# Performance work log

Hardware: AMD Instinct MI355X
Metric: run time of the kernel (lower is better)

Reference implementation:

```python
import jax, jax.numpy as jnp
import numpy as np

NUM_T = 1000   # num_timesteps == timesteps -> skip = 1, seq = range(0, 1000)
ETA = 0.1
BETA_START, BETA_END = 1e-4, 0.02


def _ddim_schedule():
    # get_beta_schedule: linspace in float64, then cast
    betas = np.linspace(BETA_START, BETA_END, NUM_T, dtype=np.float64)
    # compute_alpha prepends beta=0 -> alpha_cumprod[0] = 1.0, indexed at t+1
    alph = np.concatenate([[1.0], np.cumprod(1.0 - betas)]).astype(np.float32)
    seq = np.arange(NUM_T)
    seq_next = np.concatenate([[-1], seq[:-1]])
    at = alph[seq + 1]
    at_next = alph[seq_next + 1]   # t=-1 -> alph[0] = 1.0
    # loop iterates reversed(seq) x reversed(seq_next)
    return (jnp.asarray(at[::-1].copy()),
            jnp.asarray(at_next[::-1].copy()),
            jnp.asarray(seq[::-1].copy(), dtype=jnp.int32))


def setup_inputs() -> dict:
    key = jax.random.key(0)
    k1, k2, k3, k4, k5 = jax.random.split(key, 5)
    n, c, s, h, w = 2, 3, 8, 64, 44
    return {
        "skes": jax.random.normal(k1, (n, c, s, h, w), dtype=jnp.float32),
        "sil_T": jax.random.normal(k2, (n * s, 1, h, w), dtype=jnp.float32),
        "w_skes": jax.random.normal(k3, (c,), dtype=jnp.float32),
        "w_sil": jax.random.normal(k4, (), dtype=jnp.float32),
        "t_scale": jax.random.normal(k5, (), dtype=jnp.float32),
    }


def reference(skes, sil_T, w_skes, w_sil, t_scale):
    n, c, s, h, w = skes.shape
    # rearrange 'n c s h w -> (n s) c h w'
    skes2 = jnp.transpose(skes, (0, 2, 1, 3, 4)).reshape(n * s, c, h, w)
    # surrogate denoiser condition: 1x1 channel projection of the skeleton maps
    cond = jnp.einsum('nchw,c->nhw', skes2, w_skes)[:, None]  # (n*s,1,h,w)
    at_r, atn_r, idx_r = _ddim_schedule()
    noise_key = jax.random.key(42)

    def model(sil_t, t_val):
        t_emb = t_scale * (t_val.astype(jnp.float32) / NUM_T)
        return jnp.tanh(cond + w_sil * sil_t + t_emb)

    def step(sil_t, x):
        at, atn, idx = x
        sil_0 = model(sil_t, idx)
        # NOTE: original uses the FIXED initial noise sil_T here (not sil_t)
        et = (sil_T - jnp.sqrt(at) * sil_0) / jnp.sqrt(1.0 - at)
        c1 = ETA * jnp.sqrt((1.0 - at / atn) * (1.0 - atn) / (1.0 - at))
        c2 = jnp.sqrt(jnp.maximum(1.0 - atn - c1 * c1, 0.0))
        noise = jax.random.normal(jax.random.fold_in(noise_key, idx),
                                  sil_T.shape, dtype=sil_T.dtype)
        sil_next = jnp.sqrt(atn) * sil_0 + c1 * noise + c2 * et
        return sil_next, sil_0

    _, preds = jax.lax.scan(step, sil_T, (at_r, atn_r, idx_r))
    # preds: (1000, n*s, 1, h, w) == stacked list of per-step sil_0 predictions
    return preds
```

## Files before the change

kernel.cpp:

```cpp
#include <hip/hip_runtime.h>
#include <cstdint>

#define NSTEP 1000
#define NELEM 45056
#define HW    2816
#define EPB   64
#define PW    8
#define BLK   ((PW + 1) * 64)
#define WIN   40
#define SPP   (WIN / PW)
#define NWIN  (NSTEP / WIN)

struct AlphTab { float a[NSTEP + 1]; };

constexpr AlphTab make_alph() {
    AlphTab t{};
    t.a[0] = 1.0f;
    double alph = 1.0;
    const double start = 1e-4, stop = 0.02;
    const double step = (stop - start) / 999.0;
    for (int i = 0; i < NSTEP; ++i) {
        double beta = (i == NSTEP - 1) ? stop : ((double)i * step + start);
        alph *= (1.0 - beta);
        t.a[i + 1] = (float)alph;
    }
    return t;
}
constexpr AlphTab ALPH = make_alph();

__device__ __forceinline__ void tf20(uint32_t K0, uint32_t K1, uint32_t K2,
                                     uint32_t& x0, uint32_t& x1) {
    x0 += K0; x1 += K1;
#define TFR(r) { x0 += x1; x1 = ((x1 << r) | (x1 >> (32 - r))); x1 ^= x0; }
    TFR(13) TFR(15) TFR(26) TFR(6)
    x0 += K1; x1 += K2 + 1u;
    TFR(17) TFR(29) TFR(16) TFR(24)
    x0 += K2; x1 += K0 + 2u;
    TFR(13) TFR(15) TFR(26) TFR(6)
    x0 += K0; x1 += K1 + 3u;
    TFR(17) TFR(29) TFR(16) TFR(24)
    x0 += K1; x1 += K2 + 4u;
    TFR(13) TFR(15) TFR(26) TFR(6)
    x0 += K2; x1 += K0 + 5u;
#undef TFR
}

__device__ __forceinline__ float bits_to_erfinv(uint32_t bits) {
    const float f2 = __uint_as_float((bits >> 9) | 0x3F800000u) - 1.0f;
    const float u  = f2 * 2.0f - 0.99999994f;
    const float t1 = (1.0f - u) * (1.0f + u);
    const float w  = __log2f(t1) * -0.6931472f;
    const bool  lt = w < 5.0f;

    const float wwn = w - 2.5f;
    float pn =           2.81022636e-08f;
    pn = fmaf(pn, wwn,   3.43273939e-07f);
    pn = fmaf(pn, wwn,  -3.5233877e-06f);
    pn = fmaf(pn, wwn,  -4.39150654e-06f);
    pn = fmaf(pn, wwn,   0.00021858087f);
    pn = fmaf(pn, wwn,  -0.00125372503f);
    pn = fmaf(pn, wwn,  -0.00417768164f);
    pn = fmaf(pn, wwn,   0.246640727f);
    pn = fmaf(pn, wwn,   1.50140941f);

    float p = pn;
    if (__any(!lt)) {
        const float sw  = __builtin_amdgcn_sqrtf(w);
        const float wwf = sw - 3.0f;
        float pf =           -0.000200214257f;
        pf = fmaf(pf, wwf,    0.000100950558f);
        pf = fmaf(pf, wwf,    0.00134934322f);
        pf = fmaf(pf, wwf,   -0.00367342844f);
        pf = fmaf(pf, wwf,    0.00573950773f);
        pf = fmaf(pf, wwf,   -0.0076224613f);
        pf = fmaf(pf, wwf,    0.00943887047f);
        pf = fmaf(pf, wwf,    1.00167406f);
        pf = fmaf(pf, wwf,    2.83297682f);
        p = lt ? pn : pf;
    }
    return p * u;
}

__global__ __launch_bounds__(BLK)
void fused_kernel(const float* __restrict__ skes,
                  const float* __restrict__ silT,
                  const float* __restrict__ wskes,
                  const float* __restrict__ wsil_p,
                  const float* __restrict__ tsc_p,
                  float* __restrict__ out) {
    __shared__ __align__(16) uint4    tabP[NSTEP];
    __shared__            uint32_t    tabK2[NSTEP];
    __shared__ __align__(8)  uint2    tabC[NSTEP];
    __shared__ __align__(16) float    dbuf[2][WIN][EPB];

    const float wsil = wsil_p[0];
    const float tsc  = tsc_p[0];
    const float L2E2 = 2.8853900817779268f;

    for (int k = (int)threadIdx.x; k < NSTEP; k += BLK) {
        const int t = 999 - k;
        const float at  = ALPH.a[t + 1];
        const float atn = ALPH.a[t];
        const float c1 = 0.1f * sqrtf((1.0f - at / atn) * (1.0f - atn) / (1.0f - at));
        const float c2 = sqrtf(fmaxf(1.0f - atn - c1 * c1, 0.0f));
        const float rs = 1.0f / sqrtf(1.0f - at);
        const float A  = sqrtf(atn) - c2 * sqrtf(at) * rs;
        const float e  = c2 * rs;
        const float temb = tsc * ((float)t / 1000.0f);
        uint32_t k0 = 0u, k1 = (uint32_t)t;
        tf20(0u, 42u, 0x1BD11BDAu ^ 42u, k0, k1);
        tabP[k]  = make_uint4(__float_as_uint(c1 * 1.4142135f),
                              __float_as_uint(e), k0, k1);
        tabK2[k] = k0 ^ k1 ^ 0x1BD11BDAu;
        tabC[k]  = make_uint2(__float_as_uint(A), __float_as_uint(temb * L2E2));
    }

    const int wid  = (int)(threadIdx.x >> 6);
    const int lane = (int)(threadIdx.x & 63);
    const int j    = (int)(blockIdx.x * EPB) + lane;

    const float sT = silT[j];

    float cc2 = 0.0f, ws2 = 0.0f, sil = 0.0f;
    if (wid == PW) {
        const int ns = j / HW;
        const int hw = j - ns * HW;
        const int n  = ns >> 3;
        const int ss = ns & 7;
        const float* sk = skes + (size_t)((n * 3) * 8 + ss) * HW + hw;
        const float w0 = wskes[0], w1 = wskes[1], w2 = wskes[2];
        const float cond = fmaf(w2, sk[2 * 8 * HW], fmaf(w1, sk[8 * HW], w0 * sk[0]));
        cc2 = cond * L2E2;
        ws2 = wsil * L2E2;
        sil = sT;
    }

    __syncthreads();

    if (wid < PW) {
        float* db = &dbuf[0][0][0];
#pragma unroll
        for (int s = 0; s < SPP; ++s) {
            const int kk = wid + s * PW;
            const uint4 ta    = tabP[kk];
            const uint32_t k2 = tabK2[kk];
            uint32_t x0 = 0u, x1 = (uint32_t)j;
            tf20(ta.z, ta.w, k2, x0, x1);
            const float ei = bits_to_erfinv(x0 ^ x1);
            db[kk * EPB + lane] =
                fmaf(__uint_as_float(ta.x), ei, __uint_as_float(ta.y) * sT);
        }
    }
    __syncthreads();

    float* op = out + j;

    for (int w = 0; w < NWIN; ++w) {
        if (wid < PW) {
            if (w + 1 < NWIN) {
                float* db = &dbuf[(w + 1) & 1][0][0];
                const int kbase = (w + 1) * WIN;
#pragma unroll
                for (int s = 0; s < SPP; ++s) {
                    const int kk = wid + s * PW;
                    const int k  = kbase + kk;
                    const uint4 ta    = tabP[k];
                    const uint32_t k2 = tabK2[k];
                    uint32_t x0 = 0u, x1 = (uint32_t)j;
                    tf20(ta.z, ta.w, k2, x0, x1);
                    const float ei = bits_to_erfinv(x0 ^ x1);
                    db[kk * EPB + lane] =
                        fmaf(__uint_as_float(ta.x), ei, __uint_as_float(ta.y) * sT);
                }
            }
        } else {
            const float* db = &dbuf[w & 1][0][0];
            const int kbase = w * WIN;
#pragma unroll 4
            for (int kk = 0; kk < WIN; ++kk) {
                const uint2 tt = tabC[kbase + kk];
                const float A  = __uint_as_float(tt.x);
                const float tb = __uint_as_float(tt.y);
                const float e2 = __builtin_amdgcn_exp2f(fmaf(ws2, sil, cc2 + tb));
                const float r  = __builtin_amdgcn_rcpf(e2 + 1.0f);
                const float s0 = fmaf(-2.0f, r, 1.0f);
                *op = s0; op += NELEM;
                sil = fmaf(A, s0, db[kk * EPB + lane]);
            }
        }
        __syncthreads();
    }
}

extern "C" void kernel_launch(void* const* d_in, const int* in_sizes, int n_in,
                              void* d_out, int out_size, void* d_ws, size_t ws_size,
                              hipStream_t stream) {
    const float* skes = (const float*)d_in[0];
    const float* silT = (const float*)d_in[1];
    const float* wsk  = (const float*)d_in[2];
    const float* wsil = (const float*)d_in[3];
    const float* tsc  = (const float*)d_in[4];
    float* out = (float*)d_out;
    (void)in_sizes; (void)n_in; (void)out_size; (void)d_ws; (void)ws_size;

    dim3 grid(NELEM / EPB), block(BLK);
    hipLaunchKernelGGL(fused_kernel, grid, block, 0, stream,
                       skes, silT, wsk, wsil, tsc, out);
}
```

Measured before the change: 321.4 us.

## Replace windowed barrier pipeline with flag-based producer-consumer ring buffer

The block-wide __syncthreads double-buffered windows are replaced by a 64-slot shared-memory ring. Eight producer waves publish per-step flags, and the consumer wave polls those flags with a ballot and advances a shared consumer position. This removes barrier stalls where the serial consumer wave waits for the slowest producer, or the reverse, at every window boundary. Producers get raised priority and the tabK2 table is dropped in favour of recomputing the key. The cost is spin-wait polling, s_sleep latency, and relying on volatile LDS accesses plus block fences for ordering.

```diff
diff --git a/kernel.cpp b/kernel.cpp
--- a/kernel.cpp
+++ b/kernel.cpp
@@ -7,9 +7,7 @@
 #define EPB   64
 #define PW    8
 #define BLK   ((PW + 1) * 64)
-#define WIN   40
-#define SPP   (WIN / PW)
-#define NWIN  (NSTEP / WIN)
+#define RING  64
 
 struct AlphTab { float a[NSTEP + 1]; };
 
@@ -89,9 +87,10 @@
                   const float* __restrict__ tsc_p,
                   float* __restrict__ out) {
     __shared__ __align__(16) uint4    tabP[NSTEP];
-    __shared__            uint32_t    tabK2[NSTEP];
     __shared__ __align__(8)  uint2    tabC[NSTEP];
-    __shared__ __align__(16) float    dbuf[2][WIN][EPB];
+    __shared__ __align__(16) float    dbuf[RING][EPB];
+    __shared__ uint32_t               flags[RING];
+    __shared__ uint32_t               consPos;
 
     const float wsil = wsil_p[0];
     const float tsc  = tsc_p[0];
@@ -111,9 +110,10 @@
         tf20(0u, 42u, 0x1BD11BDAu ^ 42u, k0, k1);
         tabP[k]  = make_uint4(__float_as_uint(c1 * 1.4142135f),
                               __float_as_uint(e), k0, k1);
-        tabK2[k] = k0 ^ k1 ^ 0x1BD11BDAu;
         tabC[k]  = make_uint2(__float_as_uint(A), __float_as_uint(temb * L2E2));
     }
+    if (threadIdx.x < RING) flags[threadIdx.x] = 0u;
+    if (threadIdx.x == 0)   consPos = 0u;
 
     const int wid  = (int)(threadIdx.x >> 6);
     const int lane = (int)(threadIdx.x & 63);
@@ -138,57 +138,57 @@
     __syncthreads();
 
     if (wid < PW) {
-        float* db = &dbuf[0][0][0];
-#pragma unroll
-        for (int s = 0; s < SPP; ++s) {
-            const int kk = wid + s * PW;
-            const uint4 ta    = tabP[kk];
-            const uint32_t k2 = tabK2[kk];
-            uint32_t x0 = 0u, x1 = (uint32_t)j;
-            tf20(ta.z, ta.w, k2, x0, x1);
-            const float ei = bits_to_erfinv(x0 ^ x1);
-            db[kk * EPB + lane] =
-                fmaf(__uint_as_float(ta.x), ei, __uint_as_float(ta.y) * sT);
-        }
-    }
-    __syncthreads();
-
-    float* op = out + j;
-
-    for (int w = 0; w < NWIN; ++w) {
-        if (wid < PW) {
-            if (w + 1 < NWIN) {
-                float* db = &dbuf[(w + 1) & 1][0][0];
-                const int kbase = (w + 1) * WIN;
-#pragma unroll
-                for (int s = 0; s < SPP; ++s) {
-                    const int kk = wid + s * PW;
-                    const int k  = kbase + kk;
-                    const uint4 ta    = tabP[k];
-                    const uint32_t k2 = tabK2[k];
-                    uint32_t x0 = 0u, x1 = (uint32_t)j;
-                    tf20(ta.z, ta.w, k2, x0, x1);
-                    const float ei = bits_to_erfinv(x0 ^ x1);
-                    db[kk * EPB + lane] =
-                        fmaf(__uint_as_float(ta.x), ei, __uint_as_float(ta.y) * sT);
+        __builtin_amdgcn_s_setprio(1);
+        volatile uint32_t* vcons = &consPos;
+        int cached = 0;
+#pragma unroll 1
+        for (int k = wid; k < NSTEP; k += PW) {
+            if (k >= RING) {
+                const int need = k - RING + 1;
+                while (cached < need) {
+                    cached = (int)*vcons;
+                    if (cached < need) __builtin_amdgcn_s_sleep(1);
                 }
             }
-        } else {
-            const float* db = &dbuf[w & 1][0][0];
-            const int kbase = w * WIN;
-#pragma unroll 4
-            for (int kk = 0; kk < WIN; ++kk) {
-                const uint2 tt = tabC[kbase + kk];
+            const uint4 ta = tabP[k];
+            uint32_t x0 = 0u, x1 = (uint32_t)j;
+            tf20(ta.z, ta.w, ta.z ^ ta.w ^ 0x1BD11BDAu, x0, x1);
+            const float ei = bits_to_erfinv(x0 ^ x1);
+            dbuf[k & (RING - 1)][lane] =
+                fmaf(__uint_as_float(ta.x), ei, __uint_as_float(ta.y) * sT);
+            __threadfence_block();
+            if (lane == 0)
+                ((volatile uint32_t*)flags)[k & (RING - 1)] = (uint32_t)(k + 1);
+        }
+    } else {
+        volatile uint32_t* vflags = flags;
+        float* op = out + j;
+        int k = 0;
+        while (k < NSTEP) {
+            const int kl = k + lane;
+            bool ready = true;
+            if (kl < NSTEP)
+                ready = (vflags[kl & (RING - 1)] == (uint32_t)(kl + 1));
+            const unsigned long long m = __ballot(ready);
+            int run = (~m == 0ull) ? 64 : (__ffsll((unsigned long long)~m) - 1);
+            if (run <= 0) { __builtin_amdgcn_s_sleep(1); continue; }
+            if (run > NSTEP - k) run = NSTEP - k;
+#pragma unroll 1
+            for (int i = 0; i < run; ++i) {
+                const float d  = dbuf[(k + i) & (RING - 1)][lane];
+                const uint2 tt = tabC[k + i];
                 const float A  = __uint_as_float(tt.x);
                 const float tb = __uint_as_float(tt.y);
                 const float e2 = __builtin_amdgcn_exp2f(fmaf(ws2, sil, cc2 + tb));
                 const float r  = __builtin_amdgcn_rcpf(e2 + 1.0f);
                 const float s0 = fmaf(-2.0f, r, 1.0f);
                 *op = s0; op += NELEM;
-                sil = fmaf(A, s0, db[kk * EPB + lane]);
+                sil = fmaf(A, s0, d);
             }
+            k += run;
+            __threadfence_block();
+            if (lane == 0) *((volatile uint32_t*)&consPos) = (uint32_t)k;
         }
-        __syncthreads();
     }
 }
 
```

New measurement: 435.6 us. 1.36x slower.

## Replace block barriers with LDS counter-based producer/consumer handoff between waves

Applied to the files above, without the earlier changes.

Removes the per-window __syncthreads. Producer waves now signal window completion through atomic counters in shared memory, and the consumer wave publishes its progress position, giving asynchronous double-buffered flow control. Producers get raised scheduling priority, the K2 table is dropped in favour of recomputation, and the consumer batches LDS loads in groups of four. It relies on LDS spin-waits with volatile accesses and compiler-only memory fences, which risks ordering bugs across waves and adds spin overhead.

```diff
diff --git a/kernel.cpp b/kernel.cpp
--- a/kernel.cpp
+++ b/kernel.cpp
@@ -10,6 +10,7 @@
 #define WIN   40
 #define SPP   (WIN / PW)
 #define NWIN  (NSTEP / WIN)
+#define NBUF  2
 
 struct AlphTab { float a[NSTEP + 1]; };
 
@@ -89,9 +90,10 @@
                   const float* __restrict__ tsc_p,
                   float* __restrict__ out) {
     __shared__ __align__(16) uint4    tabP[NSTEP];
-    __shared__            uint32_t    tabK2[NSTEP];
     __shared__ __align__(8)  uint2    tabC[NSTEP];
-    __shared__ __align__(16) float    dbuf[2][WIN][EPB];
+    __shared__ __align__(16) float    dbuf[NBUF][WIN][EPB];
+    __shared__ uint32_t               wincnt[NWIN];
+    __shared__ uint32_t               consPos;
 
     const float wsil = wsil_p[0];
     const float tsc  = tsc_p[0];
@@ -111,9 +113,10 @@
         tf20(0u, 42u, 0x1BD11BDAu ^ 42u, k0, k1);
         tabP[k]  = make_uint4(__float_as_uint(c1 * 1.4142135f),
                               __float_as_uint(e), k0, k1);
-        tabK2[k] = k0 ^ k1 ^ 0x1BD11BDAu;
         tabC[k]  = make_uint2(__float_as_uint(A), __float_as_uint(temb * L2E2));
     }
+    if (threadIdx.x < NWIN) wincnt[threadIdx.x] = 0u;
+    if (threadIdx.x == 0)   consPos = 0u;
 
     const int wid  = (int)(threadIdx.x >> 6);
     const int lane = (int)(threadIdx.x & 63);
@@ -138,57 +141,65 @@
     __syncthreads();
 
     if (wid < PW) {
-        float* db = &dbuf[0][0][0];
-#pragma unroll
-        for (int s = 0; s < SPP; ++s) {
-            const int kk = wid + s * PW;
-            const uint4 ta    = tabP[kk];
-            const uint32_t k2 = tabK2[kk];
-            uint32_t x0 = 0u, x1 = (uint32_t)j;
-            tf20(ta.z, ta.w, k2, x0, x1);
-            const float ei = bits_to_erfinv(x0 ^ x1);
-            db[kk * EPB + lane] =
-                fmaf(__uint_as_float(ta.x), ei, __uint_as_float(ta.y) * sT);
+        __builtin_amdgcn_s_setprio(1);
+        volatile uint32_t* vcons = &consPos;
+#pragma unroll 1
+        for (int w = 0; w < NWIN; ++w) {
+            if (w >= NBUF) {
+                const uint32_t need = (uint32_t)(w - NBUF + 1);
+                while (*vcons < need) __builtin_amdgcn_s_sleep(2);
+            }
+            const int kbase = w * WIN + wid;
+            uint4 tt[SPP];
+#pragma unroll
+            for (int s = 0; s < SPP; ++s) tt[s] = tabP[kbase + s * PW];
+            float* db = &dbuf[w & (NBUF - 1)][0][0];
+#pragma unroll
+            for (int s = 0; s < SPP; ++s) {
+                uint32_t x0 = 0u, x1 = (uint32_t)j;
+                tf20(tt[s].z, tt[s].w, tt[s].z ^ tt[s].w ^ 0x1BD11BDAu, x0, x1);
+                const float ei = bits_to_erfinv(x0 ^ x1);
+                db[(wid + s * PW) * EPB + lane] =
+                    fmaf(__uint_as_float(tt[s].x), ei,
+                         __uint_as_float(tt[s].y) * sT);
+            }
+            asm volatile("" ::: "memory");
+            if (lane == 0) atomicAdd(&wincnt[w], 1u);
+            asm volatile("" ::: "memory");
         }
-    }
-    __syncthreads();
-
-    float* op = out + j;
-
-    for (int w = 0; w < NWIN; ++w) {
-        if (wid < PW) {
-            if (w + 1 < NWIN) {
-                float* db = &dbuf[(w + 1) & 1][0][0];
-                const int kbase = (w + 1) * WIN;
-#pragma unroll
-                for (int s = 0; s < SPP; ++s) {
-                    const int kk = wid + s * PW;
-                    const int k  = kbase + kk;
-                    const uint4 ta    = tabP[k];
-                    const uint32_t k2 = tabK2[k];
-                    uint32_t x0 = 0u, x1 = (uint32_t)j;
-                    tf20(ta.z, ta.w, k2, x0, x1);
-                    const float ei = bits_to_erfinv(x0 ^ x1);
-                    db[kk * EPB + lane] =
-                        fmaf(__uint_as_float(ta.x), ei, __uint_as_float(ta.y) * sT);
+    } else {
+        volatile uint32_t* vwin  = wincnt;
+        volatile uint32_t* vcons = &consPos;
+        float* op = out + j;
+#pragma unroll 1
+        for (int w = 0; w < NWIN; ++w) {
+            while (vwin[w] < (uint32_t)PW) __builtin_amdgcn_s_sleep(1);
+            asm volatile("" ::: "memory");
+            const float* db = &dbuf[w & (NBUF - 1)][0][0];
+            const int kbase = w * WIN;
+#pragma unroll 1
+            for (int g = 0; g < WIN / 4; ++g) {
+                float d4[4]; uint2 t4[4];
+#pragma unroll
+                for (int i = 0; i < 4; ++i) {
+                    d4[i] = db[(g * 4 + i) * EPB + lane];
+                    t4[i] = tabC[kbase + g * 4 + i];
+                }
+#pragma unroll
+                for (int i = 0; i < 4; ++i) {
+                    const float A  = __uint_as_float(t4[i].x);
+                    const float tb = __uint_as_float(t4[i].y);
+                    const float e2 = __builtin_amdgcn_exp2f(fmaf(ws2, sil, cc2 + tb));
+                    const float r  = __builtin_amdgcn_rcpf(e2 + 1.0f);
+                    const float s0 = fmaf(-2.0f, r, 1.0f);
+                    *op = s0; op += NELEM;
+                    sil = fmaf(A, s0, d4[i]);
                 }
             }
-        } else {
-            const float* db = &dbuf[w & 1][0][0];
-            const int kbase = w * WIN;
-#pragma unroll 4
-            for (int kk = 0; kk < WIN; ++kk) {
-                const uint2 tt = tabC[kbase + kk];
-                const float A  = __uint_as_float(tt.x);
-                const float tb = __uint_as_float(tt.y);
-                const float e2 = __builtin_amdgcn_exp2f(fmaf(ws2, sil, cc2 + tb));
-                const float r  = __builtin_amdgcn_rcpf(e2 + 1.0f);
-                const float s0 = fmaf(-2.0f, r, 1.0f);
-                *op = s0; op += NELEM;
-                sil = fmaf(A, s0, db[kk * EPB + lane]);
-            }
+            asm volatile("" ::: "memory");
+            *vcons = (uint32_t)(w + 1);
+            asm volatile("" ::: "memory");
         }
-        __syncthreads();
     }
 }
 
```

Result: slower. 349.6 us (+8.8%).

## Move step tables to a setup kernel in workspace and shrink producer warps

Applied to the files above, without the earlier changes.

A separate setup kernel now precomputes the per-step coefficient and RNG-key tables into global workspace, so each block no longer rebuilds them in shared memory. That frees most of the LDS, which together with 7 producer waves and a launch-bounds occupancy hint is meant to let more blocks run per CU. The consumer wave batches its loads of 8 buffer entries and table values before running the serial tanh chain, and a monolithic fallback kernel is added for when the workspace is too small. The cost is an extra kernel launch and global or cache reads of the tables in place of LDS reads.

```diff
diff --git a/kernel.cpp b/kernel.cpp
--- a/kernel.cpp
+++ b/kernel.cpp
@@ -5,11 +5,13 @@
 #define NELEM 45056
 #define HW    2816
 #define EPB   64
-#define PW    8
+#define PW    7
 #define BLK   ((PW + 1) * 64)
 #define WIN   40
-#define SPP   (WIN / PW)
 #define NWIN  (NSTEP / WIN)
+#define NBUF  2
+#define TABC_OFF 16384
+#define WS_NEED  (TABC_OFF + NSTEP * 8)
 
 struct AlphTab { float a[NSTEP + 1]; };
 
@@ -45,6 +47,12 @@
 #undef TFR
 }
 
+__device__ __forceinline__ float fast_tanh(float x) {
+    const float e2 = __expf(x + x);
+    const float r  = __builtin_amdgcn_rcpf(e2 + 1.0f);
+    return fmaf(-2.0f, r, 1.0f);
+}
+
 __device__ __forceinline__ float bits_to_erfinv(uint32_t bits) {
     const float f2 = __uint_as_float((bits >> 9) | 0x3F800000u) - 1.0f;
     const float u  = f2 * 2.0f - 0.99999994f;
@@ -81,23 +89,127 @@
     return p * u;
 }
 
-__global__ __launch_bounds__(BLK)
+__global__ __launch_bounds__(256)
+void setup_kernel(const float* __restrict__ tsc_p,
+                  uint4* __restrict__ tabPg, uint2* __restrict__ tabCg) {
+    const int k = (int)(blockIdx.x * 256u + threadIdx.x);
+    if (k >= NSTEP) return;
+    const float tsc = tsc_p[0];
+    const float L2E2 = 2.8853900817779268f;
+    const int t = 999 - k;
+    const float at  = ALPH.a[t + 1];
+    const float atn = ALPH.a[t];
+    const float c1 = 0.1f * sqrtf((1.0f - at / atn) * (1.0f - atn) / (1.0f - at));
+    const float c2 = sqrtf(fmaxf(1.0f - atn - c1 * c1, 0.0f));
+    const float rs = 1.0f / sqrtf(1.0f - at);
+    const float A  = sqrtf(atn) - c2 * sqrtf(at) * rs;
+    const float e  = c2 * rs;
+    const float temb = tsc * ((float)t / 1000.0f);
+    uint32_t k0 = 0u, k1 = (uint32_t)t;
+    tf20(0u, 42u, 0x1BD11BDAu ^ 42u, k0, k1);
+    tabPg[k] = make_uint4(__float_as_uint(c1 * 1.4142135f),
+                          __float_as_uint(e), k0, k1);
+    tabCg[k] = make_uint2(__float_as_uint(A), __float_as_uint(temb * L2E2));
+}
+
+__device__ __forceinline__ void produce_window(const uint4* __restrict__ tabPg,
+                                               float* __restrict__ db,
+                                               int kbase, int wid, int lane,
+                                               int j, float sT) {
+    const int ks0 = __builtin_amdgcn_readfirstlane(kbase + wid);
+#pragma unroll 2
+    for (int s = 0, kk = wid; kk < WIN; ++s, kk += PW) {
+        const uint4 ta = tabPg[ks0 + s * PW];
+        uint32_t x0 = 0u, x1 = (uint32_t)j;
+        tf20(ta.z, ta.w, ta.z ^ ta.w ^ 0x1BD11BDAu, x0, x1);
+        const float ei = bits_to_erfinv(x0 ^ x1);
+        db[kk * EPB + lane] =
+            fmaf(__uint_as_float(ta.x), ei, __uint_as_float(ta.y) * sT);
+    }
+}
+
+__global__ __launch_bounds__(BLK, 8)
 void fused_kernel(const float* __restrict__ skes,
                   const float* __restrict__ silT,
                   const float* __restrict__ wskes,
                   const float* __restrict__ wsil_p,
-                  const float* __restrict__ tsc_p,
+                  const uint4* __restrict__ tabPg,
+                  const uint2* __restrict__ tabCg,
                   float* __restrict__ out) {
-    __shared__ __align__(16) uint4    tabP[NSTEP];
-    __shared__            uint32_t    tabK2[NSTEP];
-    __shared__ __align__(8)  uint2    tabC[NSTEP];
-    __shared__ __align__(16) float    dbuf[2][WIN][EPB];
-
+    __shared__ __align__(16) float dbuf[NBUF][WIN][EPB];
+
+    const int wid  = (int)(threadIdx.x >> 6);
+    const int lane = (int)(threadIdx.x & 63);
+    const int j    = (int)(blockIdx.x * EPB) + lane;
+
+    const float sT = silT[j];
+
+    float cc2 = 0.0f, ws2 = 0.0f, sil = 0.0f;
+    if (wid == PW) {
+        const float L2E2 = 2.8853900817779268f;
+        const int ns = j / HW;
+        const int hw = j - ns * HW;
+        const int n  = ns >> 3;
+        const int ss = ns & 7;
+        const float* sk = skes + (size_t)((n * 3) * 8 + ss) * HW + hw;
+        const float w0 = wskes[0], w1 = wskes[1], w2 = wskes[2];
+        const float cond = fmaf(w2, sk[2 * 8 * HW], fmaf(w1, sk[8 * HW], w0 * sk[0]));
+        cc2 = cond * L2E2;
+        ws2 = wsil_p[0] * L2E2;
+        sil = sT;
+    }
+
+    if (wid < PW) {
+        produce_window(tabPg, &dbuf[0][0][0], 0, wid, lane, j, sT);
+    }
+    __syncthreads();
+
+    float* op = out + j;
+
+    for (int w = 0; w < NWIN; ++w) {
+        if (wid < PW) {
+            if (w + 1 < NWIN) {
+                produce_window(tabPg, &dbuf[(w + 1) & (NBUF - 1)][0][0],
+                               (w + 1) * WIN, wid, lane, j, sT);
+            }
+        } else {
+            const float* db = &dbuf[w & (NBUF - 1)][0][0];
+            const int ks0 = __builtin_amdgcn_readfirstlane(w * WIN);
+#pragma unroll 1
+            for (int g = 0; g < WIN / 8; ++g) {
+                float d8[8]; uint2 t8[8];
+#pragma unroll
+                for (int i = 0; i < 8; ++i) {
+                    d8[i] = db[(g * 8 + i) * EPB + lane];
+                    t8[i] = tabCg[ks0 + g * 8 + i];
+                }
+#pragma unroll
+                for (int i = 0; i < 8; ++i) {
+                    const float A  = __uint_as_float(t8[i].x);
+                    const float tb = __uint_as_float(t8[i].y);
+                    const float e2 = __builtin_amdgcn_exp2f(fmaf(ws2, sil, cc2 + tb));
+                    const float r  = __builtin_amdgcn_rcpf(e2 + 1.0f);
+                    const float s0 = fmaf(-2.0f, r, 1.0f);
+                    *op = s0; op += NELEM;
+                    sil = fmaf(A, s0, d8[i]);
+                }
+            }
+        }
+        __syncthreads();
+    }
+}
+
+__global__ __launch_bounds__(256)
+void diffgait_mono(const float* __restrict__ skes,
+                   const float* __restrict__ silT,
+                   const float* __restrict__ wskes,
+                   const float* __restrict__ wsil_p,
+                   const float* __restrict__ tsc_p,
+                   float* __restrict__ out) {
+    __shared__ __align__(16) uint32_t tab[NSTEP][8];
     const float wsil = wsil_p[0];
     const float tsc  = tsc_p[0];
-    const float L2E2 = 2.8853900817779268f;
-
-    for (int k = (int)threadIdx.x; k < NSTEP; k += BLK) {
+    for (int k = (int)threadIdx.x; k < NSTEP; k += 256) {
         const int t = 999 - k;
         const float at  = ALPH.a[t + 1];
         const float atn = ALPH.a[t];
@@ -107,88 +219,40 @@
         const float A  = sqrtf(atn) - c2 * sqrtf(at) * rs;
         const float e  = c2 * rs;
         const float temb = tsc * ((float)t / 1000.0f);
-        uint32_t k0 = 0u, k1 = (uint32_t)t;
-        tf20(0u, 42u, 0x1BD11BDAu ^ 42u, k0, k1);
-        tabP[k]  = make_uint4(__float_as_uint(c1 * 1.4142135f),
-                              __float_as_uint(e), k0, k1);
-        tabK2[k] = k0 ^ k1 ^ 0x1BD11BDAu;
-        tabC[k]  = make_uint2(__float_as_uint(A), __float_as_uint(temb * L2E2));
-    }
-
-    const int wid  = (int)(threadIdx.x >> 6);
-    const int lane = (int)(threadIdx.x & 63);
-    const int j    = (int)(blockIdx.x * EPB) + lane;
-
+        uint32_t x0 = 0u, x1 = (uint32_t)t;
+        tf20(0u, 42u, 0x1BD11BDAu ^ 42u, x0, x1);
+        tab[k][0] = __float_as_uint(A);
+        tab[k][1] = __float_as_uint(temb);
+        tab[k][2] = __float_as_uint(c1 * 1.4142135f);
+        tab[k][3] = __float_as_uint(e);
+        tab[k][4] = x0;
+        tab[k][5] = x1;
+        tab[k][6] = x0 ^ x1 ^ 0x1BD11BDAu;
+        tab[k][7] = 0u;
+    }
+    __syncthreads();
+    const int j  = (int)(blockIdx.x * 256u + threadIdx.x);
+    const int ns = j / HW;
+    const int hw = j - ns * HW;
+    const int n  = ns >> 3;
+    const int ss = ns & 7;
+    const float* sk = skes + (size_t)((n * 3) * 8 + ss) * HW + hw;
+    const float w0 = wskes[0], w1 = wskes[1], w2 = wskes[2];
+    const float cond = fmaf(w2, sk[2 * 8 * HW], fmaf(w1, sk[8 * HW], w0 * sk[0]));
     const float sT = silT[j];
-
-    float cc2 = 0.0f, ws2 = 0.0f, sil = 0.0f;
-    if (wid == PW) {
-        const int ns = j / HW;
-        const int hw = j - ns * HW;
-        const int n  = ns >> 3;
-        const int ss = ns & 7;
-        const float* sk = skes + (size_t)((n * 3) * 8 + ss) * HW + hw;
-        const float w0 = wskes[0], w1 = wskes[1], w2 = wskes[2];
-        const float cond = fmaf(w2, sk[2 * 8 * HW], fmaf(w1, sk[8 * HW], w0 * sk[0]));
-        cc2 = cond * L2E2;
-        ws2 = wsil * L2E2;
-        sil = sT;
-    }
-
-    __syncthreads();
-
-    if (wid < PW) {
-        float* db = &dbuf[0][0][0];
-#pragma unroll
-        for (int s = 0; s < SPP; ++s) {
-            const int kk = wid + s * PW;
-            const uint4 ta    = tabP[kk];
-            const uint32_t k2 = tabK2[kk];
-            uint32_t x0 = 0u, x1 = (uint32_t)j;
-            tf20(ta.z, ta.w, k2, x0, x1);
-            const float ei = bits_to_erfinv(x0 ^ x1);
-            db[kk * EPB + lane] =
-                fmaf(__uint_as_float(ta.x), ei, __uint_as_float(ta.y) * sT);
-        }
-    }
-    __syncthreads();
-
+    float sil = sT;
     float* op = out + j;
-
-    for (int w = 0; w < NWIN; ++w) {
-        if (wid < PW) {
-            if (w + 1 < NWIN) {
-                float* db = &dbuf[(w + 1) & 1][0][0];
-                const int kbase = (w + 1) * WIN;
-#pragma unroll
-                for (int s = 0; s < SPP; ++s) {
-                    const int kk = wid + s * PW;
-                    const int k  = kbase + kk;
-                    const uint4 ta    = tabP[k];
-                    const uint32_t k2 = tabK2[k];
-                    uint32_t x0 = 0u, x1 = (uint32_t)j;
-                    tf20(ta.z, ta.w, k2, x0, x1);
-                    const float ei = bits_to_erfinv(x0 ^ x1);
-                    db[kk * EPB + lane] =
-                        fmaf(__uint_as_float(ta.x), ei, __uint_as_float(ta.y) * sT);
-                }
-            }
-        } else {
-            const float* db = &dbuf[w & 1][0][0];
-            const int kbase = w * WIN;
-#pragma unroll 4
-            for (int kk = 0; kk < WIN; ++kk) {
-                const uint2 tt = tabC[kbase + kk];
-                const float A  = __uint_as_float(tt.x);
-                const float tb = __uint_as_float(tt.y);
-                const float e2 = __builtin_amdgcn_exp2f(fmaf(ws2, sil, cc2 + tb));
-                const float r  = __builtin_amdgcn_rcpf(e2 + 1.0f);
-                const float s0 = fmaf(-2.0f, r, 1.0f);
-                *op = s0; op += NELEM;
-                sil = fmaf(A, s0, db[kk * EPB + lane]);
-            }
-        }
-        __syncthreads();
+#pragma unroll 2
+    for (int k = 0; k < NSTEP; ++k) {
+        const uint4 ta = *(const uint4*)&tab[k][0];
+        const uint4 tb = *(const uint4*)&tab[k][4];
+        uint32_t x0 = 0u, x1 = (uint32_t)j;
+        tf20(tb.x, tb.y, tb.z, x0, x1);
+        const float ei = bits_to_erfinv(x0 ^ x1);
+        const float d  = fmaf(__uint_as_float(ta.z), ei, __uint_as_float(ta.w) * sT);
+        const float s0 = fast_tanh(fmaf(wsil, sil, cond) + __uint_as_float(ta.y));
+        *op = s0; op += NELEM;
+        sil = fmaf(__uint_as_float(ta.x), s0, d);
     }
 }
 
@@ -201,9 +265,19 @@
     const float* wsil = (const float*)d_in[3];
     const float* tsc  = (const float*)d_in[4];
     float* out = (float*)d_out;
-    (void)in_sizes; (void)n_in; (void)out_size; (void)d_ws; (void)ws_size;
-
-    dim3 grid(NELEM / EPB), block(BLK);
-    hipLaunchKernelGGL(fused_kernel, grid, block, 0, stream,
-                       skes, silT, wsk, wsil, tsc, out);
-}
+    (void)in_sizes; (void)n_in; (void)out_size;
+
+    if (ws_size >= (size_t)WS_NEED) {
+        uint4* tabPg = (uint4*)d_ws;
+        uint2* tabCg = (uint2*)((char*)d_ws + TABC_OFF);
+        hipLaunchKernelGGL(setup_kernel, dim3(4), dim3(256), 0, stream,
+                           tsc, tabPg, tabCg);
+        dim3 grid(NELEM / EPB), block(BLK);
+        hipLaunchKernelGGL(fused_kernel, grid, block, 0, stream,
+                           skes, silT, wsk, wsil, tabPg, tabCg, out);
+    } else {
+        dim3 grid(NELEM / 256), block(256);
+        hipLaunchKernelGGL(diffgait_mono, grid, block, 0, stream,
+                           skes, silT, wsk, wsil, tsc, out);
+    }
+}
```

Result: faster. 294.2 us (-8.5%).
